# Kernel optimization log

Hardware: AMD Instinct MI355X
Metric: run time of the kernel (lower is better)

Reference implementation:

```python
import jax, jax.numpy as jnp
import numpy as np

E = 8       # n_experts
K = 2       # k_experts
D_IN = 1024
D_OUT = 1024
D_EXP = 2048
N = 16384   # tokens (batch*seq, forward requires 2D input)


def setup_inputs() -> dict:
    key = jax.random.key(0)
    ks = jax.random.split(key, 4)
    x = jax.random.normal(ks[0], (N, D_IN), jnp.float32)
    Wg = jax.random.normal(ks[1], (E, D_IN), jnp.float32) * 0.02      # router weight
    bg = jnp.zeros((E,), jnp.float32)                                  # router bias
    W_in = jax.random.normal(ks[2], (E, D_EXP, D_IN), jnp.float32) * 0.02
    b_in = jnp.zeros((E, D_EXP), jnp.float32)                          # w_in_bias_init=0.0
    W_out = jax.random.normal(ks[3], (E, D_OUT, D_EXP), jnp.float32) * 0.02  # bias=False
    return {"x": x, "Wg": Wg, "bg": bg, "W_in": W_in, "b_in": b_in, "W_out": W_out}


def moe_forward(x, Wg, bg, W_in, b_in, W_out):
    # Eval mode: gate jitter / solu jitter / dropouts are training-only no-ops.
    n = x.shape[0]
    # --- routing ---
    logits = x @ Wg.T + bg                                 # [N, E]
    probs = jax.nn.softmax(logits, axis=-1)
    mean_probs = probs.mean(axis=0)                        # [E]
    k_vals, k_idx = jax.lax.top_k(probs, K)                # [N, K]
    k_w = k_vals / k_vals.sum(axis=-1, keepdims=True)      # renormalized gate weights
    counts = jnp.bincount(k_idx.reshape(-1), length=E)     # [E] int
    load_balancing_loss = E * jnp.sum((counts.astype(x.dtype) / n) * mean_probs)
    # --- dispatch + expert w_in (loop over fixed small E; combine with one-hot mask) ---
    sel = jax.nn.one_hot(k_idx, E, dtype=x.dtype)          # [N, K, E]
    h = jnp.zeros((n, K, D_EXP), x.dtype)                  # preacts per (token, slot)
    for e in range(E):
        he = x @ W_in[e].T + b_in[e]                       # [N, D_EXP]
        h = h + sel[:, :, e][..., None] * he[:, None, :]
    # --- SoLU (eval): softmax(preacts) * preacts over hidden dim ---
    acts = jax.nn.softmax(h, axis=-1) * h                  # [N, K, D_EXP]
    # --- expert w_out (no bias) ---
    out = jnp.zeros((n, K, D_OUT), x.dtype)
    for e in range(E):
        oe = jnp.einsum('nkh,oh->nko', acts, W_out[e])
        out = out + sel[:, :, e][..., None] * oe
    # --- weighted combine over the K chosen experts ---
    outputs = (out * k_w[..., None]).sum(axis=1)           # [N, D_OUT]
    return outputs, load_balancing_loss


def reference(x, Wg, bg, W_in, b_in, W_out):
    return moe_forward(x, Wg, bg, W_in, b_in, W_out)
```

## Files before the change

### kernel.cpp

```cpp
#include <hip/hip_runtime.h>
#include <hip/hip_bf16.h>
#include <stdint.h>

#define E_EXP 8
#define NTOK  16384
#define DIN   1024
#define DEXP  2048
#define DOUT  1024
#define NSLOT (NTOK*2)
#define MAXT  136

#define TS_T  (256*64)

typedef __attribute__((ext_vector_type(8))) short short8;
typedef __attribute__((ext_vector_type(8))) unsigned short ushort8;
typedef __attribute__((ext_vector_type(4))) unsigned short ushort4v;
typedef __attribute__((ext_vector_type(4))) float f32x4;

__device__ __forceinline__ unsigned short f2bf(float f){
  union { float f; uint32_t u; } v; v.f = f;
  uint32_t r = (v.u + 0x7FFFu + ((v.u >> 16) & 1u)) >> 16;
  return (unsigned short)r;
}
__device__ __forceinline__ float bf2f(unsigned short u){
  union { uint32_t u; float f; } v; v.u = ((uint32_t)u) << 16;
  return v.f;
}

__device__ __forceinline__ void async16(const void* g, void* l){
  __builtin_amdgcn_global_load_lds(
      (const __attribute__((address_space(1))) void*)g,
      (__attribute__((address_space(3))) void*)l, 16, 0, 0);
}

#define VMCNT0()  asm volatile("s_waitcnt vmcnt(0)"  ::: "memory")
#define BARRIER() do { asm volatile("" ::: "memory"); __builtin_amdgcn_s_barrier(); asm volatile("" ::: "memory"); } while(0)

__global__ __launch_bounds__(256) void cast2(const float* __restrict__ a,
                                             const float* __restrict__ b,
                                             unsigned short* __restrict__ da,
                                             unsigned short* __restrict__ db,
                                             int na, int nb){
  int i = (blockIdx.x*256 + threadIdx.x)*8;
  const float* s; unsigned short* d;
  if (i < na){ s = a + i; d = da + i; }
  else { int j = i - na; if (j >= nb) return; s = b + j; d = db + j; }
  float4 x = *(const float4*)(s);
  float4 y = *(const float4*)(s+4);
  ushort8 o;
  o[0]=f2bf(x.x); o[1]=f2bf(x.y); o[2]=f2bf(x.z); o[3]=f2bf(x.w);
  o[4]=f2bf(y.x); o[5]=f2bf(y.y); o[6]=f2bf(y.z); o[7]=f2bf(y.w);
  *(ushort8*)d = o;
}

__global__ __launch_bounds__(256) void router(
    const float* __restrict__ x, const float* __restrict__ Wg, const float* __restrict__ bg,
    unsigned short* __restrict__ xb,
    int* __restrict__ eidx, float* __restrict__ gw,
    int* __restrict__ counts, float* __restrict__ probsum)
{
  __shared__ float sWg[E_EXP*DIN];
  __shared__ float sps[E_EXP];
  __shared__ int   scnt[E_EXP];
  const int tid = threadIdx.x;
  for (int i = tid; i < E_EXP*DIN; i += 256) sWg[i] = Wg[i];
  if (tid < E_EXP){ sps[tid]=0.f; scnt[tid]=0; }
  __syncthreads();
  const int lane = tid & 63;
  const int wv   = tid >> 6;
  for (int it = 0; it < 16; ++it){
    const int token = blockIdx.x*64 + wv*16 + it;
    float4 xv[4];
#pragma unroll
    for (int j=0;j<4;++j) xv[j] = *(const float4*)&x[(size_t)token*DIN + j*256 + lane*4];
#pragma unroll
    for (int j=0;j<4;++j){
      ushort4v o;
      o[0]=f2bf(xv[j].x); o[1]=f2bf(xv[j].y); o[2]=f2bf(xv[j].z); o[3]=f2bf(xv[j].w);
      *(ushort4v*)&xb[(size_t)token*DIN + j*256 + lane*4] = o;
    }
    float p[E_EXP];
#pragma unroll
    for (int e2=0;e2<E_EXP;++e2){
      float s = 0.f;
#pragma unroll
      for (int j=0;j<4;++j){
        const float4 w4 = *(const float4*)&sWg[e2*DIN + j*256 + lane*4];
        s += xv[j].x*w4.x + xv[j].y*w4.y + xv[j].z*w4.z + xv[j].w*w4.w;
      }
      p[e2] = s;
    }
#pragma unroll
    for (int d=1; d<64; d<<=1){
#pragma unroll
      for (int e2=0;e2<E_EXP;++e2) p[e2] += __shfl_xor(p[e2], d);
    }
    if (lane == 0){
      float mx = -1e30f;
#pragma unroll
      for (int e2=0;e2<E_EXP;++e2){ p[e2] += bg[e2]; mx = fmaxf(mx, p[e2]); }
      float se = 0.f;
#pragma unroll
      for (int e2=0;e2<E_EXP;++e2){ p[e2] = __expf(p[e2]-mx); se += p[e2]; }
      const float inv = 1.f/se;
#pragma unroll
      for (int e2=0;e2<E_EXP;++e2){ p[e2] *= inv; atomicAdd(&sps[e2], p[e2]); }
      int i1 = 0;
#pragma unroll
      for (int e2=1;e2<E_EXP;++e2) if (p[e2] > p[i1]) i1 = e2;
      int i2 = (i1==0) ? 1 : 0;
#pragma unroll
      for (int e2=0;e2<E_EXP;++e2) if (e2 != i1 && p[e2] > p[i2]) i2 = e2;
      const float v1 = p[i1], v2 = p[i2], s12 = v1 + v2;
      eidx[2*token]   = i1; eidx[2*token+1] = i2;
      gw[2*token]     = v1/s12; gw[2*token+1] = v2/s12;
      atomicAdd(&scnt[i1], 1); atomicAdd(&scnt[i2], 1);
    }
  }
  __syncthreads();
  if (tid < E_EXP){ atomicAdd(&counts[tid], scnt[tid]); atomicAdd(&probsum[tid], sps[tid]); }
}

__global__ void finalize(const int* __restrict__ counts, const float* __restrict__ probsum,
                         float* __restrict__ loss_out, int* __restrict__ offs,
                         int* __restrict__ cursor, int* __restrict__ tile_e,
                         int* __restrict__ tile_row, int* __restrict__ ntiles)
{
  const int lane = threadIdx.x;
  int c[E_EXP];
#pragma unroll
  for (int e=0;e<E_EXP;++e) c[e] = counts[e];
  int off[E_EXP+1], tb[E_EXP+1];
  off[0]=0; tb[0]=0;
#pragma unroll
  for (int e=0;e<E_EXP;++e){ off[e+1]=off[e]+c[e]; tb[e+1]=tb[e]+((c[e]+255)>>8); }
  if (lane==0){
    float loss=0.f;
#pragma unroll
    for (int e=0;e<E_EXP;++e) loss += (float)c[e]*probsum[e];
    *loss_out = loss * (8.f/((float)NTOK*(float)NTOK));
    *ntiles = tb[E_EXP];
    offs[E_EXP] = off[E_EXP];
  }
  if (lane < E_EXP){ cursor[lane]=0; offs[lane]=off[lane]; }
  const int nt = tb[E_EXP];
  for (int i=lane; i<nt; i+=64){
    int e=0;
#pragma unroll
    for (int k=0;k<E_EXP-1;++k) if (i >= tb[k+1]) e = k+1;
    tile_e[i]   = e;
    tile_row[i] = off[e] + (i - tb[e])*256;
  }
}

__global__ __launch_bounds__(256) void scatter(const int* __restrict__ eidx,
    const float* __restrict__ gw,
    const int* __restrict__ offs, int* __restrict__ cursor,
    int* __restrict__ ptok, float* __restrict__ pw)
{
  const int t = blockIdx.x*256 + threadIdx.x;
  if (t >= NTOK) return;
#pragma unroll
  for (int s=0;s<2;++s){
    const int e2  = eidx[2*t+s];
    const int pos = offs[e2] + atomicAdd(&cursor[e2], 1);
    ptok[pos] = t;
    pw[pos]   = gw[2*t+s];
  }
}

#define STAGE8(buf, ko) do {                                              \
  async16(ag[0]+(ko),  &As[buf][L0]);  async16(ag[1]+(ko),  &As[buf][L1]);\
  async16(ag[2]+(ko),  &As[buf][L2o]); async16(ag[3]+(ko),  &As[buf][L3]);\
  async16(bg4[0]+(ko), &Bs[buf][L0]);  async16(bg4[1]+(ko), &Bs[buf][L1]);\
  async16(bg4[2]+(ko), &Bs[buf][L2o]); async16(bg4[3]+(ko), &Bs[buf][L3]);} while(0)

__global__ __launch_bounds__(512) void gemm1(
    const unsigned short* __restrict__ xb,
    const unsigned short* __restrict__ wib,
    const float* __restrict__ b_in,
    unsigned short* __restrict__ H,
    const int* __restrict__ ptok,
    const int* __restrict__ offs,
    const int* __restrict__ tile_e,
    const int* __restrict__ tile_row,
    const int* __restrict__ ntiles)
{
  const int gid   = (int)blockIdx.y * 8 + (int)blockIdx.x;
  const int rank  = (gid & 7) * 136 + (gid >> 3);
  const int rtile = rank >> 3;
  const int panel = rank & 7;
  if (rtile >= *ntiles) return;
  const int e    = tile_e[rtile];
  const int row0 = tile_row[rtile];
  const int seg_end = offs[e+1];
  const int col0 = panel * 256;

  __shared__ unsigned short As[2][TS_T];
  __shared__ unsigned short Bs[2][TS_T];

  const int tid  = threadIdx.x;
  const int lane = tid & 63;
  const int wv   = tid >> 6;
  const int wm   = wv >> 2;
  const int wn   = wv & 3;
  const int srow = tid >> 3;
  const int scol = ((tid & 7) ^ (srow & 7)) * 8;

  const unsigned short* ag[4];
#pragma unroll
  for (int i = 0; i < 4; ++i){
    int g = row0 + i*64 + srow; if (g > NSLOT-1) g = NSLOT-1;
    const int tok = ptok[g];
    ag[i] = xb + (size_t)tok*DIN + scol;
  }
  const unsigned short* bg4[4];
#pragma unroll
  for (int i = 0; i < 4; ++i)
    bg4[i] = wib + ((size_t)e*DEXP + col0 + i*64 + srow)*DIN + scol;
  float bias[4];
#pragma unroll
  for (int n = 0; n < 4; ++n)
    bias[n] = b_in[e*DEXP + col0 + wn*64 + n*16 + (lane&15)];

  f32x4 acc[8][4] = {};
  const int NK = DIN/64;
  int cur = 0;

  const unsigned int L0 = (wv*8)*64, L1 = (64+wv*8)*64, L2o = (128+wv*8)*64, L3 = (192+wv*8)*64;

  STAGE8(0, 0);
  VMCNT0();
  BARRIER();

  for (int kt = 0; kt < NK; ++kt){
    if (kt + 1 < NK) STAGE8(cur^1, (kt+1)*64);

    __builtin_amdgcn_s_setprio(1);
#pragma unroll
    for (int kk = 0; kk < 2; ++kk){
      const int ksl = ((kk*4 + (lane>>4)) ^ (lane & 7)) * 8;
      short8 a[8], b[4];
#pragma unroll
      for (int m = 0; m < 8; ++m)
        a[m] = *(const short8*)&As[cur][(wm*128 + m*16 + (lane&15))*64 + ksl];
#pragma unroll
      for (int n = 0; n < 4; ++n)
        b[n] = *(const short8*)&Bs[cur][(wn*64 + n*16 + (lane&15))*64 + ksl];
#pragma unroll
      for (int m = 0; m < 8; ++m)
#pragma unroll
        for (int n = 0; n < 4; ++n)
          acc[m][n] = __builtin_amdgcn_mfma_f32_16x16x32_bf16(a[m], b[n], acc[m][n], 0, 0, 0);
    }
    __builtin_amdgcn_s_setprio(0);

    VMCNT0();
    BARRIER();
    cur ^= 1;
  }

#pragma unroll
  for (int m = 0; m < 8; ++m){
#pragma unroll
    for (int j = 0; j < 4; ++j){
      const int r = wm*128 + m*16 + (lane>>4)*4 + j;
      const int g = row0 + r;
      if (g < seg_end){
#pragma unroll
        for (int n = 0; n < 4; ++n){
          const int c = col0 + wn*64 + n*16 + (lane&15);
          H[(size_t)g*DEXP + c] = f2bf(acc[m][n][j] + bias[n]);
        }
      }
    }
  }
}

__global__ __launch_bounds__(256) void solu(unsigned short* __restrict__ H){
  const size_t row = blockIdx.x;
  unsigned short* hp = H + row*DEXP;
  const int tid  = threadIdx.x;
  const int lane = tid & 63;
  const int wv   = tid >> 6;
  const short8 hv = *(const short8*)&hp[tid*8];
  float f[8];
#pragma unroll
  for (int j=0;j<8;++j) f[j] = bf2f((unsigned short)hv[j]);
  float mx = f[0];
#pragma unroll
  for (int j=1;j<8;++j) mx = fmaxf(mx, f[j]);
  for (int d=1; d<64; d<<=1) mx = fmaxf(mx, __shfl_xor(mx, d));
  __shared__ float redm[4];
  __shared__ float reds[4];
  if (lane==0) redm[wv] = mx;
  __syncthreads();
  mx = fmaxf(fmaxf(redm[0],redm[1]), fmaxf(redm[2],redm[3]));
  float se = 0.f; float ex[8];
#pragma unroll
  for (int j=0;j<8;++j){ ex[j] = __expf(f[j]-mx); se += ex[j]; }
  for (int d=1; d<64; d<<=1) se += __shfl_xor(se, d);
  if (lane==0) reds[wv] = se;
  __syncthreads();
  se = reds[0]+reds[1]+reds[2]+reds[3];
  const float inv = 1.0f/se;
  ushort8 o;
#pragma unroll
  for (int j=0;j<8;++j) o[j] = f2bf(f[j]*ex[j]*inv);
  *(ushort8*)&hp[tid*8] = o;
}

__global__ __launch_bounds__(512) void gemm2(
    const unsigned short* __restrict__ ACT,
    const unsigned short* __restrict__ wob,
    float* __restrict__ out,
    const int* __restrict__ ptok,
    const float* __restrict__ pw,
    const int* __restrict__ offs,
    const int* __restrict__ tile_e,
    const int* __restrict__ tile_row,
    const int* __restrict__ ntiles)
{
  const int gid   = (int)blockIdx.y * 4 + (int)blockIdx.x;
  const int rank  = (gid & 7) * 68 + (gid >> 3);
  const int rtile = rank >> 2;
  const int panel = rank & 3;
  if (rtile >= *ntiles) return;
  const int e    = tile_e[rtile];
  const int row0 = tile_row[rtile];
  const int seg_end = offs[e+1];
  const int col0 = panel * 256;

  __shared__ unsigned short As[2][TS_T];
  __shared__ unsigned short Bs[2][TS_T];

  const int tid  = threadIdx.x;
  const int lane = tid & 63;
  const int wv   = tid >> 6;
  const int wm   = wv >> 2;
  const int wn   = wv & 3;
  const int srow = tid >> 3;
  const int scol = ((tid & 7) ^ (srow & 7)) * 8;

  const unsigned short* ag[4];
#pragma unroll
  for (int i = 0; i < 4; ++i){
    int g = row0 + i*64 + srow; if (g > NSLOT-1) g = NSLOT-1;
    ag[i] = ACT + (size_t)g*DEXP + scol;
  }
  const unsigned short* bg4[4];
#pragma unroll
  for (int i = 0; i < 4; ++i)
    bg4[i] = wob + ((size_t)e*DOUT + col0 + i*64 + srow)*DEXP + scol;

  f32x4 acc[8][4] = {};
  const int NK = DEXP/64;
  int cur = 0;

  const unsigned int L0 = (wv*8)*64, L1 = (64+wv*8)*64, L2o = (128+wv*8)*64, L3 = (192+wv*8)*64;

  STAGE8(0, 0);
  VMCNT0();
  BARRIER();

  for (int kt = 0; kt < NK; ++kt){
    if (kt + 1 < NK) STAGE8(cur^1, (kt+1)*64);

    __builtin_amdgcn_s_setprio(1);
#pragma unroll
    for (int kk = 0; kk < 2; ++kk){
      const int ksl = ((kk*4 + (lane>>4)) ^ (lane & 7)) * 8;
      short8 a[8], b[4];
#pragma unroll
      for (int m = 0; m < 8; ++m)
        a[m] = *(const short8*)&As[cur][(wm*128 + m*16 + (lane&15))*64 + ksl];
#pragma unroll
      for (int n = 0; n < 4; ++n)
        b[n] = *(const short8*)&Bs[cur][(wn*64 + n*16 + (lane&15))*64 + ksl];
#pragma unroll
      for (int m = 0; m < 8; ++m)
#pragma unroll
        for (int n = 0; n < 4; ++n)
          acc[m][n] = __builtin_amdgcn_mfma_f32_16x16x32_bf16(a[m], b[n], acc[m][n], 0, 0, 0);
    }
    __builtin_amdgcn_s_setprio(0);

    VMCNT0();
    BARRIER();
    cur ^= 1;
  }

#pragma unroll
  for (int m = 0; m < 8; ++m){
#pragma unroll
    for (int j = 0; j < 4; ++j){
      const int r = wm*128 + m*16 + (lane>>4)*4 + j;
      const int g = row0 + r;
      if (g < seg_end){
        const int tok   = ptok[g];
        const float wgt = pw[g];
        float* op = out + (size_t)tok*DOUT;
#pragma unroll
        for (int n = 0; n < 4; ++n){
          const int c = col0 + wn*64 + n*16 + (lane&15);
          unsafeAtomicAdd(op + c, wgt * acc[m][n][j]);
        }
      }
    }
  }
}

extern "C" void kernel_launch(void* const* d_in, const int* in_sizes, int n_in,
                              void* d_out, int out_size, void* d_ws, size_t ws_size,
                              hipStream_t stream)
{
  const float* x     = (const float*)d_in[0];
  const float* Wg    = (const float*)d_in[1];
  const float* bgp   = (const float*)d_in[2];
  const float* W_in  = (const float*)d_in[3];
  const float* b_in  = (const float*)d_in[4];
  const float* W_out = (const float*)d_in[5];
  float* out = (float*)d_out;

  char* base = (char*)d_ws;
  size_t o = 0;
  unsigned short* xb  = (unsigned short*)(base + o); o += (size_t)NTOK*DIN*2;
  unsigned short* wib = (unsigned short*)(base + o); o += (size_t)E_EXP*DEXP*DIN*2;
  unsigned short* wob = (unsigned short*)(base + o); o += (size_t)E_EXP*DOUT*DEXP*2;
  unsigned short* H   = (unsigned short*)(base + o); o += (size_t)NSLOT*DEXP*2;
  int*   eidx    = (int*)(base + o);   o += (size_t)NSLOT*4;
  float* gw      = (float*)(base + o); o += (size_t)NSLOT*4;
  int*   ptok    = (int*)(base + o);   o += (size_t)NSLOT*4;
  float* pw      = (float*)(base + o); o += (size_t)NSLOT*4;
  int*   counts  = (int*)(base + o);   o += 32;
  float* probsum = (float*)(base + o); o += 32;
  int*   cursor  = (int*)(base + o);   o += 32;
  int*   offs    = (int*)(base + o);   o += 64;
  int*   tile_e  = (int*)(base + o);   o += (size_t)MAXT*4;
  int*   tile_row= (int*)(base + o);   o += (size_t)MAXT*4;
  int*   ntiles  = (int*)(base + o);   o += 64;

  hipMemsetAsync(d_out, 0, (size_t)NTOK*DOUT*4 + 4, stream);
  hipMemsetAsync(counts, 0, 96, stream);

  cast2<<<dim3(16384), 256, 0, stream>>>(W_in, W_out, wib, wob,
                                         E_EXP*DEXP*DIN, E_EXP*DOUT*DEXP);

  router<<<dim3(256), 256, 0, stream>>>(x, Wg, bgp, xb, eidx, gw, counts, probsum);
  finalize<<<dim3(1), 64, 0, stream>>>(counts, probsum, out + (size_t)NTOK*DOUT,
                                       offs, cursor, tile_e, tile_row, ntiles);
  scatter<<<dim3(64), 256, 0, stream>>>(eidx, gw, offs, cursor, ptok, pw);

  gemm1<<<dim3(DEXP/256, MAXT), 512, 0, stream>>>(xb, wib, b_in, H, ptok, offs,
                                                  tile_e, tile_row, ntiles);
  solu<<<dim3(NSLOT), 256, 0, stream>>>(H);
  gemm2<<<dim3(DOUT/256, MAXT), 512, 0, stream>>>(H, wob, out, ptok, pw, offs,
                                                  tile_e, tile_row, ntiles);
}
```

Baseline: 805.7 us.

## Restructure GEMM load pipelines with partial vmcnt waits and interleaved staging

In gemm1, the next-tile async loads are now issued after a top-of-loop barrier and followed by a partial vmcnt wait (vmcnt(8)), so the wait for each stage happens just before compute. gemm2 gets a deeper pipeline: B and part of A for tile k+2 are prefetched into the buffer currently being consumed. The MFMA work is split into four phases, and the prefetch loads are spread across those phases with barriers between them. The goal is to overlap global-to-LDS traffic with MFMA work and avoid full vmcnt(0) stalls. The cost is many more barriers per k-step, plus a correctness risk from the hand-counted vmcnt values and from overwriting a buffer that is still being read.

Result: no change. 795.4 us (-1.3%).

```diff
diff --git a/kernel.cpp b/kernel.cpp
--- a/kernel.cpp
+++ b/kernel.cpp
@@ -33,7 +33,10 @@
       (__attribute__((address_space(3))) void*)l, 16, 0, 0);
 }
 
+#define VMCNT8()  asm volatile("s_waitcnt vmcnt(8)"  ::: "memory")
+#define VMCNT6()  asm volatile("s_waitcnt vmcnt(6)"  ::: "memory")
 #define VMCNT0()  asm volatile("s_waitcnt vmcnt(0)"  ::: "memory")
+#define LGKM0()   asm volatile("s_waitcnt lgkmcnt(0)" ::: "memory")
 #define BARRIER() do { asm volatile("" ::: "memory"); __builtin_amdgcn_s_barrier(); asm volatile("" ::: "memory"); } while(0)
 
 __global__ __launch_bounds__(256) void cast2(const float* __restrict__ a,
@@ -168,12 +171,6 @@
     pw[pos]   = gw[2*t+s];
   }
 }
-
-#define STAGE8(buf, ko) do {                                              \
-  async16(ag[0]+(ko),  &As[buf][L0]);  async16(ag[1]+(ko),  &As[buf][L1]);\
-  async16(ag[2]+(ko),  &As[buf][L2o]); async16(ag[3]+(ko),  &As[buf][L3]);\
-  async16(bg4[0]+(ko), &Bs[buf][L0]);  async16(bg4[1]+(ko), &Bs[buf][L1]);\
-  async16(bg4[2]+(ko), &Bs[buf][L2o]); async16(bg4[3]+(ko), &Bs[buf][L3]);} while(0)
 
 __global__ __launch_bounds__(512) void gemm1(
     const unsigned short* __restrict__ xb,
@@ -229,12 +226,24 @@
 
   const unsigned int L0 = (wv*8)*64, L1 = (64+wv*8)*64, L2o = (128+wv*8)*64, L3 = (192+wv*8)*64;
 
-  STAGE8(0, 0);
-  VMCNT0();
-  BARRIER();
+  async16(ag[0],  &As[0][L0]);  async16(ag[1],  &As[0][L1]);
+  async16(ag[2],  &As[0][L2o]); async16(ag[3],  &As[0][L3]);
+  async16(bg4[0], &Bs[0][L0]);  async16(bg4[1], &Bs[0][L1]);
+  async16(bg4[2], &Bs[0][L2o]); async16(bg4[3], &Bs[0][L3]);
 
   for (int kt = 0; kt < NK; ++kt){
-    if (kt + 1 < NK) STAGE8(cur^1, (kt+1)*64);
+    BARRIER();
+    if (kt + 1 < NK){
+      const int ko = (kt+1)*64;
+      async16(ag[0]  + ko, &As[cur^1][L0]);  async16(ag[1]  + ko, &As[cur^1][L1]);
+      async16(ag[2]  + ko, &As[cur^1][L2o]); async16(ag[3]  + ko, &As[cur^1][L3]);
+      async16(bg4[0] + ko, &Bs[cur^1][L0]);  async16(bg4[1] + ko, &Bs[cur^1][L1]);
+      async16(bg4[2] + ko, &Bs[cur^1][L2o]); async16(bg4[3] + ko, &Bs[cur^1][L3]);
+      VMCNT8();
+    } else {
+      VMCNT0();
+    }
+    BARRIER();
 
     __builtin_amdgcn_s_setprio(1);
 #pragma unroll
@@ -254,9 +263,6 @@
           acc[m][n] = __builtin_amdgcn_mfma_f32_16x16x32_bf16(a[m], b[n], acc[m][n], 0, 0, 0);
     }
     __builtin_amdgcn_s_setprio(0);
-
-    VMCNT0();
-    BARRIER();
     cur ^= 1;
   }
 
@@ -359,34 +365,89 @@
 
   const unsigned int L0 = (wv*8)*64, L1 = (64+wv*8)*64, L2o = (128+wv*8)*64, L3 = (192+wv*8)*64;
 
-  STAGE8(0, 0);
-  VMCNT0();
+  async16(bg4[0], &Bs[0][L0]);  async16(bg4[1], &Bs[0][L1]);
+  async16(bg4[2], &Bs[0][L2o]); async16(bg4[3], &Bs[0][L3]);
+  async16(ag[0],  &As[0][L0]);  async16(ag[1],  &As[0][L1]);
+  async16(ag[2],  &As[0][L2o]); async16(ag[3],  &As[0][L3]);
+  async16(bg4[0]+64, &Bs[1][L0]);  async16(bg4[1]+64, &Bs[1][L1]);
+  async16(bg4[2]+64, &Bs[1][L2o]); async16(bg4[3]+64, &Bs[1][L3]);
+  async16(ag[0]+64,  &As[1][L0]);  async16(ag[2]+64,  &As[1][L2o]);
+  VMCNT6();
   BARRIER();
 
   for (int kt = 0; kt < NK; ++kt){
-    if (kt + 1 < NK) STAGE8(cur^1, (kt+1)*64);
-
-    __builtin_amdgcn_s_setprio(1);
-#pragma unroll
-    for (int kk = 0; kk < 2; ++kk){
-      const int ksl = ((kk*4 + (lane>>4)) ^ (lane & 7)) * 8;
-      short8 a[8], b[4];
-#pragma unroll
-      for (int m = 0; m < 8; ++m)
-        a[m] = *(const short8*)&As[cur][(wm*128 + m*16 + (lane&15))*64 + ksl];
-#pragma unroll
-      for (int n = 0; n < 4; ++n)
-        b[n] = *(const short8*)&Bs[cur][(wn*64 + n*16 + (lane&15))*64 + ksl];
-#pragma unroll
-      for (int m = 0; m < 8; ++m)
+    const bool s1 = (kt + 1 < NK);
+    const bool s2 = (kt + 2 < NK);
+    const int koN  = (kt+1)*64;
+    const int koNN = (kt+2)*64;
+    unsigned short* Acur = &As[cur][0];
+    unsigned short* Bcur = &Bs[cur][0];
+    unsigned short* Anxt = &As[cur^1][0];
+    const int k0 = (((lane>>4))   ^ (lane & 7)) * 8;
+    const int k1 = ((4+(lane>>4)) ^ (lane & 7)) * 8;
+
+    short8 b0[4], b1[4];
+
+    {
+      short8 a0_[2], a1_[2];
+#pragma unroll
+      for (int n = 0; n < 4; ++n){
+        const int rr = (wn*64 + n*16 + (lane&15))*64;
+        b0[n] = *(const short8*)&Bcur[rr + k0];
+        b1[n] = *(const short8*)&Bcur[rr + k1];
+      }
+#pragma unroll
+      for (int i = 0; i < 2; ++i){
+        const int rr = (wm*128 + i*16 + (lane&15))*64;
+        a0_[i] = *(const short8*)&Acur[rr + k0];
+        a1_[i] = *(const short8*)&Acur[rr + k1];
+      }
+      if (s1){ async16(ag[1]+koN, Anxt+L1); async16(ag[3]+koN, Anxt+L3); }
+      BARRIER(); LGKM0();
+      __builtin_amdgcn_s_setprio(1);
+#pragma unroll
+      for (int i = 0; i < 2; ++i)
 #pragma unroll
         for (int n = 0; n < 4; ++n)
-          acc[m][n] = __builtin_amdgcn_mfma_f32_16x16x32_bf16(a[m], b[n], acc[m][n], 0, 0, 0);
-    }
-    __builtin_amdgcn_s_setprio(0);
-
-    VMCNT0();
-    BARRIER();
+          acc[i][n] = __builtin_amdgcn_mfma_f32_16x16x32_bf16(a0_[i], b0[n], acc[i][n], 0, 0, 0);
+#pragma unroll
+      for (int i = 0; i < 2; ++i)
+#pragma unroll
+        for (int n = 0; n < 4; ++n)
+          acc[i][n] = __builtin_amdgcn_mfma_f32_16x16x32_bf16(a1_[i], b1[n], acc[i][n], 0, 0, 0);
+      __builtin_amdgcn_s_setprio(0);
+      BARRIER();
+    }
+#pragma unroll
+    for (int p = 1; p < 4; ++p){
+      short8 a0_[2], a1_[2];
+#pragma unroll
+      for (int i = 0; i < 2; ++i){
+        const int rr = (wm*128 + (p*2+i)*16 + (lane&15))*64;
+        a0_[i] = *(const short8*)&Acur[rr + k0];
+        a1_[i] = *(const short8*)&Acur[rr + k1];
+      }
+      if (s2){
+        if (p == 1){ async16(bg4[0]+koNN, Bcur+L0);  async16(bg4[1]+koNN, Bcur+L1);  }
+        if (p == 2){ async16(bg4[2]+koNN, Bcur+L2o); async16(bg4[3]+koNN, Bcur+L3);  }
+        if (p == 3){ async16(ag[0]+koNN,  Acur+L0);  async16(ag[2]+koNN,  Acur+L2o); }
+      }
+      BARRIER(); LGKM0();
+      __builtin_amdgcn_s_setprio(1);
+#pragma unroll
+      for (int i = 0; i < 2; ++i)
+#pragma unroll
+        for (int n = 0; n < 4; ++n)
+          acc[p*2+i][n] = __builtin_amdgcn_mfma_f32_16x16x32_bf16(a0_[i], b0[n], acc[p*2+i][n], 0, 0, 0);
+#pragma unroll
+      for (int i = 0; i < 2; ++i)
+#pragma unroll
+        for (int n = 0; n < 4; ++n)
+          acc[p*2+i][n] = __builtin_amdgcn_mfma_f32_16x16x32_bf16(a1_[i], b1[n], acc[p*2+i][n], 0, 0, 0);
+      __builtin_amdgcn_s_setprio(0);
+      if (p == 3){ if (s2) { VMCNT6(); } else if (s1) { VMCNT0(); } }
+      BARRIER();
+    }
     cur ^= 1;
   }
 
```
